# Optimization experiments

Hardware: AMD Instinct MI355X
Metric: run time of the kernel (lower is better)

## Reference

```python
import jax, jax.numpy as jnp
import numpy as np

E, M, T, H, V = 512, 1024, 1024, 512, 10000
B, S, L = 16, 80, 200
K = 10  # pooling kernel


def avgpool2d(x, k):
    # torch AvgPool2d(k) on a 3D tensor [B, S, C]: pools over (S, C) with stride k, floor mode
    b, s, c = x.shape
    return x[:, :(s // k) * k, :(c // k) * k].reshape(b, s // k, k, c // k, k).mean(axis=(2, 4))


def lstm(x, h0, c0, Wih, Whh, bih, bhh):
    # torch single-layer LSTM, gate order (i, f, g, o); x: [B, T, H]
    def step(carry, xt):
        h, c = carry
        g = xt @ Wih.T + h @ Whh.T + bih + bhh  # [B, 4H]
        i, f, gg, o = jnp.split(g, 4, axis=-1)
        c = jax.nn.sigmoid(f) * c + jax.nn.sigmoid(i) * jnp.tanh(gg)
        h = jax.nn.sigmoid(o) * jnp.tanh(c)
        return (h, c), h
    (hT, cT), ys = jax.lax.scan(step, (h0, c0), jnp.swapaxes(x, 0, 1))
    return jnp.swapaxes(ys, 0, 1), (hT, cT)


def attend(emb, feats, lens, Ws, bs, hdim):
    # additive score: Linear(cat(emb, feat)) = emb@We.T + feat@Wf.T + b, masked softmax over valid feats
    we, wf = Ws[:, :hdim], Ws[:, hdim:]
    scores = emb @ we.T + jnp.swapaxes(feats @ wf.T, 1, 2) + bs  # [B, S, L]
    mask = jnp.arange(feats.shape[1])[None, None, :] < lens[:, None, None]
    w = jax.nn.softmax(jnp.where(mask, scores, -jnp.inf), axis=-1)
    return jnp.einsum('bsl,blf->bsf', w, feats)


def setup_inputs():
    key = jax.random.key(0)
    ks = jax.random.split(key, 30)
    n = lambda k, shape: jax.random.normal(k, shape, dtype=jnp.float32)
    p = lambda k, shape: 0.02 * jax.random.normal(k, shape, dtype=jnp.float32)
    inp = {
        'mfeat': n(ks[0], (B, L, M)),
        'tfeat': n(ks[1], (B, L, T)),
        'att_motion': n(ks[2], (B, S, M)),
        'att_tempo': n(ks[3], (B, S, T)),
        'embeddings': n(ks[4], (B, S, E)),
        'motion_batch_lens': jax.random.randint(ks[5], (B,), 100, L + 1, dtype=jnp.int32),
        'temp_batch_lens': jax.random.randint(ks[6], (B,), 100, L + 1, dtype=jnp.int32),
        'seq_batch_lens': jnp.full((B,), S, dtype=jnp.int32),
        'Wm': p(ks[7], (M, M)), 'bm': p(ks[8], (M,)),
        'Wt': p(ks[9], (T, T)), 'bt': p(ks[10], (T,)),
        'Wmm': p(ks[11], (H, E + T + M)), 'bmm': p(ks[12], (H,)),
        'Wli': p(ks[13], (H, T // K + M // K)), 'bli': p(ks[14], (H,)),
        'Wih': p(ks[15], (4 * H, H)), 'Whh': p(ks[16], (4 * H, H)),
        'bih': p(ks[17], (4 * H,)), 'bhh': p(ks[18], (4 * H,)),
        'Wsm': p(ks[19], (1, H + M)), 'bsm': p(ks[20], (1,)),
        'Wst': p(ks[21], (1, H + T)), 'bst': p(ks[22], (1,)),
        'Wo': p(ks[23], (V, H + T + M)), 'bo': p(ks[24], (V,)),
    }
    return inp


def reference(mfeat, tfeat, att_motion, att_tempo, embeddings,
              motion_batch_lens, temp_batch_lens, seq_batch_lens,
              Wm, bm, Wt, bt, Wmm, bmm, Wli, bli,
              Wih, Whh, bih, bhh, Wsm, bsm, Wst, bst, Wo, bo):
    # self-gated feature transforms
    temp_mout = att_motion @ Wm.T + bm
    temp_tout = att_tempo @ Wt.T + bt
    temp_mout = temp_mout * jax.nn.softmax(temp_mout, axis=-1)
    temp_tout = temp_tout * jax.nn.softmax(temp_tout, axis=-1)
    # multimodal fusion (dropout = identity in eval)
    mm_inp = jnp.concatenate((embeddings, temp_tout, temp_mout), axis=2)
    mm_out = mm_inp @ Wmm.T + bmm  # [B, S, H]
    # pooled init sequence -> LSTM init hidden
    mean_feat = jnp.concatenate((avgpool2d(att_tempo, K), avgpool2d(att_motion, K)), axis=2)
    m0 = mean_feat @ Wli.T + bli  # [B, S//K, H]
    z = jnp.zeros((att_motion.shape[0], H), dtype=mm_out.dtype)
    _, (h0, c0) = lstm(m0, z, z, Wih, Whh, bih, bhh)
    out, _ = lstm(mm_out, h0, c0, Wih, Whh, bih, bhh)
    act = jnp.tanh(out)
    # ragged additive attention over variable-length video features
    att_m2 = attend(act, mfeat, motion_batch_lens, Wsm, bsm, H)
    att_t2 = attend(act, tfeat, temp_batch_lens, Wst, bst, H)
    final = jnp.concatenate((act, att_t2, att_m2), axis=2) @ Wo.T + bo
    return jax.nn.log_softmax(final, axis=2)
```

## Files before the change

kernel.cpp:

```cpp
#include <hip/hip_runtime.h>
#include <hip/hip_bf16.h>
#include <math.h>


typedef __bf16 bf16x8 __attribute__((ext_vector_type(8)));
typedef float f32x4 __attribute__((ext_vector_type(4)));
typedef unsigned short u16x8 __attribute__((ext_vector_type(8)));

__device__ inline unsigned short f2b(float f){
  union { float f; unsigned u; } v; v.f = f;
  unsigned u = v.u;
  u += 0x7fff + ((u >> 16) & 1);
  return (unsigned short)(u >> 16);
}
__device__ inline float sigm(float x){ return 1.f/(1.f + __expf(-x)); }
__device__ inline float wred_max(float v){ for (int o=32;o;o>>=1) v = fmaxf(v, __shfl_xor(v,o)); return v; }
__device__ inline float wred_sum(float v){ for (int o=32;o;o>>=1) v += __shfl_xor(v,o); return v; }

__device__ inline float bred_max(float v, float* sm){
  v = wred_max(v);
  int w = threadIdx.x >> 6;
  if ((threadIdx.x & 63) == 0) sm[w] = v;
  __syncthreads();
  v = fmaxf(fmaxf(sm[0], sm[1]), fmaxf(sm[2], sm[3]));
  __syncthreads();
  return v;
}
__device__ inline float bred_sum(float v, float* sm){
  v = wred_sum(v);
  int w = threadIdx.x >> 6;
  if ((threadIdx.x & 63) == 0) sm[w] = v;
  __syncthreads();
  v = sm[0] + sm[1] + sm[2] + sm[3];
  __syncthreads();
  return v;
}

#define GLOAD_LDS16(g, l) __builtin_amdgcn_global_load_lds( \
    (const __attribute__((address_space(1))) void*)(g), \
    (__attribute__((address_space(3))) void*)(l), 16, 0, 0)

__global__ void cvt_bf16_kernel(const float* __restrict__ s, unsigned short* __restrict__ d, int n8){
  int i = blockIdx.x*256 + threadIdx.x;
  if (i >= n8) return;
  float4 a = ((const float4*)s)[i*2];
  float4 b = ((const float4*)s)[i*2+1];
  u16x8 o;
  o[0]=f2b(a.x); o[1]=f2b(a.y); o[2]=f2b(a.z); o[3]=f2b(a.w);
  o[4]=f2b(b.x); o[5]=f2b(b.y); o[6]=f2b(b.z); o[7]=f2b(b.w);
  ((u16x8*)d)[i] = o;
}

__global__ void zero_kernel(int* p, int n){
  int i = blockIdx.x*64 + threadIdx.x;
  if (i < n) p[i] = 0;
}

__device__ __forceinline__ void gemm_body(
    const unsigned short* __restrict__ A, const unsigned short* __restrict__ B,
    const float* __restrict__ bias1, const float* __restrict__ bias2,
    float* __restrict__ C, int N, int K,
    unsigned short* lA, unsigned short* lB)
{
  int tid = threadIdx.x;
  int r0 = blockIdx.x << 7, n0 = blockIdx.y << 7;
  int w = tid >> 6, lane = tid & 63;
  int wr = (w >> 1) << 6, wc = (w & 1) << 6;
  int lm = lane & 15, lq = lane >> 4;
  f32x4 acc[4][4] = {};

  int row0 = tid >> 2, row1 = (tid + 256) >> 2, cc = (tid & 3) << 3;
  const unsigned short* Ag0 = A + (size_t)(r0 + row0)*K + cc;
  const unsigned short* Ag1 = A + (size_t)(r0 + row1)*K + cc;
  int br0 = n0 + row0; if (br0 >= N) br0 = N - 1;
  int br1 = n0 + row1; if (br1 >= N) br1 = N - 1;
  const unsigned short* Bg0 = B + (size_t)br0*K + cc;
  const unsigned short* Bg1 = B + (size_t)br1*K + cc;
  unsigned lb0 = (unsigned)(tid & ~63) * 8;
  unsigned lb1 = 2048 + lb0;

  for (int k0 = 0; k0 < K; k0 += 32){
    GLOAD_LDS16(Ag0 + k0, &lA[lb0]);
    GLOAD_LDS16(Ag1 + k0, &lA[lb1]);
    GLOAD_LDS16(Bg0 + k0, &lB[lb0]);
    GLOAD_LDS16(Bg1 + k0, &lB[lb1]);
    __syncthreads();
    bf16x8 af[4], bfr[4];
#pragma unroll
    for (int i=0;i<4;i++){
      af[i]  = *(const bf16x8*)&lA[(wr + i*16 + lm)*32 + lq*8];
      bfr[i] = *(const bf16x8*)&lB[(wc + i*16 + lm)*32 + lq*8];
    }
#pragma unroll
    for (int i=0;i<4;i++)
#pragma unroll
      for (int j=0;j<4;j++)
        acc[i][j] = __builtin_amdgcn_mfma_f32_16x16x32_bf16(af[i], bfr[j], acc[i][j], 0, 0, 0);
    __syncthreads();
  }
#pragma unroll
  for (int i=0;i<4;i++){
    int rbase = r0 + wr + i*16 + lq*4;
#pragma unroll
    for (int j=0;j<4;j++){
      int n = n0 + wc + j*16 + lm;
      if (n < N){
        float bv = (bias1 ? bias1[n] : 0.f) + (bias2 ? bias2[n] : 0.f);
#pragma unroll
        for (int rr=0;rr<4;rr++)
          C[(size_t)(rbase + rr)*N + n] = acc[i][j][rr] + bv;
      }
    }
  }
}

__global__ __launch_bounds__(256) void gemm_bb_kernel(
    const unsigned short* __restrict__ A, const unsigned short* __restrict__ B,
    const float* __restrict__ bias1, const float* __restrict__ bias2,
    float* __restrict__ C, int N, int K)
{
  __shared__ unsigned short lA[128*32];
  __shared__ unsigned short lB[128*32];
  gemm_body(A, B, bias1, bias2, C, N, K, lA, lB);
}

__global__ __launch_bounds__(256) void gemm_bb2_kernel(
    const unsigned short* __restrict__ A0, const unsigned short* __restrict__ B0,
    const float* __restrict__ b0, float* __restrict__ C0,
    const unsigned short* __restrict__ A1, const unsigned short* __restrict__ B1,
    const float* __restrict__ b1, float* __restrict__ C1, int N, int K)
{
  __shared__ unsigned short lA[128*32];
  __shared__ unsigned short lB[128*32];
  if (blockIdx.z == 0) gemm_body(A0, B0, b0, nullptr, C0, N, K, lA, lB);
  else                 gemm_body(A1, B1, b1, nullptr, C1, N, K, lA, lB);
}

__global__ __launch_bounds__(256) void rowsmx2_kernel(const float* __restrict__ X0,
    const float* __restrict__ X1, unsigned short* __restrict__ out)
{
  __shared__ float sm[4];
  int bx = blockIdx.x, tid = threadIdx.x;
  int row = (bx < 1280) ? bx : bx - 1280;
  const float* xr = ((bx < 1280) ? X0 : X1) + (size_t)row * 1024;
  int ooff = (bx < 1280) ? 1536 : 512;
  float x[4];
#pragma unroll
  for (int j=0;j<4;j++) x[j] = xr[j*256 + tid];
  float m = fmaxf(fmaxf(x[0],x[1]), fmaxf(x[2],x[3]));
  m = bred_max(m, sm);
  float s = 0.f;
#pragma unroll
  for (int j=0;j<4;j++) s += __expf(x[j]-m);
  s = bred_sum(s, sm);
  float inv = 1.f / s;
  unsigned short* o = out + (size_t)row*2560 + ooff;
#pragma unroll
  for (int j=0;j<4;j++) o[j*256 + tid] = f2b(x[j] * (__expf(x[j]-m) * inv));
}

__global__ void embcopy_kernel(const float* __restrict__ emb, unsigned short* __restrict__ mmbf){
  int idx = blockIdx.x*256 + threadIdx.x;
  if (idx >= 1280*64) return;
  int row = idx >> 6, c8 = (idx & 63) << 3;
  const float* s = emb + (size_t)row*512 + c8;
  float4 a = ((const float4*)s)[0], b = ((const float4*)s)[1];
  u16x8 o;
  o[0]=f2b(a.x); o[1]=f2b(a.y); o[2]=f2b(a.z); o[3]=f2b(a.w);
  o[4]=f2b(b.x); o[5]=f2b(b.y); o[6]=f2b(b.z); o[7]=f2b(b.w);
  *(u16x8*)&mmbf[(size_t)row*2560 + c8] = o;
}

__global__ void avgpool_kernel(const float* __restrict__ tempo, const float* __restrict__ motion,
                               float* __restrict__ mf)
{
  int bx = blockIdx.x;
  int c = threadIdx.x;
  if (c >= 204) return;
  int b = bx >> 3, s = bx & 7;
  const float* src = (c < 102) ? (tempo  + ((size_t)(b*80 + s*10))*1024 + c*10)
                               : (motion + ((size_t)(b*80 + s*10))*1024 + (c-102)*10);
  float acc = 0.f;
  for (int r=0;r<10;r++){
    const float* p = src + (size_t)r*1024;
#pragma unroll
    for (int cc=0;cc<10;cc++) acc += p[cc];
  }
  mf[bx*204 + c] = acc * 0.01f;
}

__global__ __launch_bounds__(256) void m0_kernel(const float* __restrict__ mf,
    const float* __restrict__ Wli, const float* __restrict__ bli, float* __restrict__ m0)
{
  __shared__ float rowv[204];
  int bx = blockIdx.x, tid = threadIdx.x;
  if (tid < 204) rowv[tid] = mf[bx*204 + tid];
  __syncthreads();
  for (int c = tid; c < 512; c += 256){
    const float* w = Wli + (size_t)c*204;
    float acc = bli[c];
    for (int k=0;k<204;k++) acc += rowv[k]*w[k];
    m0[bx*512 + c] = acc;
  }
}

#define LSTM_NBLK 32
#define HP 520

__global__ __launch_bounds__(256) void lstm_fused_kernel(
    const float* __restrict__ X1, const float* __restrict__ X2,
    const float* __restrict__ Whh,
    unsigned long long* __restrict__ hb0, unsigned long long* __restrict__ hb1,
    float* __restrict__ finalA, unsigned short* __restrict__ finalA_bf,
    int* __restrict__ bar,
    const float* __restrict__ Wo, unsigned short* __restrict__ Wo_bf,
    const float* __restrict__ mfeat, const float* __restrict__ tfeat,
    const float* __restrict__ Wsm, const float* __restrict__ Wst,
    float* __restrict__ f_m, float* __restrict__ f_t)
{
  __shared__ unsigned short w_lds[64*HP];
  __shared__ unsigned short h_lds[16*HP];
  __shared__ float gb[4][16][16];
  __shared__ unsigned short hstage[16][16];
  int tid = threadIdx.x, j = blockIdx.x;

  if (j >= LSTM_NBLK){
    int hb = j - LSTM_NBLK;
    for (int ch = hb*256 + tid; ch < 3200000; ch += 224*256){
      float4 a = ((const float4*)Wo)[ch*2];
      float4 b = ((const float4*)Wo)[ch*2+1];
      u16x8 o;
      o[0]=f2b(a.x); o[1]=f2b(a.y); o[2]=f2b(a.z); o[3]=f2b(a.w);
      o[4]=f2b(b.x); o[5]=f2b(b.y); o[6]=f2b(b.z); o[7]=f2b(b.w);
      ((u16x8*)Wo_bf)[ch] = o;
    }
    int wv = hb*4 + (tid >> 6);
    int lane = tid & 63;
    for (int r = wv; r < 6400; r += 896){
      const float* a = (r < 3200) ? (mfeat + (size_t)r*1024) : (tfeat + (size_t)(r-3200)*1024);
      const float* wvec = (r < 3200) ? (Wsm + 512) : (Wst + 512);
      float acc = 0.f;
      for (int c = lane; c < 1024; c += 64) acc += a[c]*wvec[c];
      acc = wred_sum(acc);
      if (lane == 0){ if (r < 3200) f_m[r] = acc; else f_t[r-3200] = acc; }
    }
    return;
  }

  int j16 = j*16;
  int lane = tid & 63, w = tid >> 6;
  int lm = lane & 15, lq = lane >> 4;

  for (int i = 0; i < 16; i++){
    int ch = tid + i*256;
    int r = ch >> 6, c8 = (ch & 63) << 3;
    int grow = (r >> 4)*512 + j16 + (r & 15);
    const float* s = Whh + (size_t)grow*512 + c8;
    float4 a = ((const float4*)s)[0], b = ((const float4*)s)[1];
    u16x8 o;
    o[0]=f2b(a.x); o[1]=f2b(a.y); o[2]=f2b(a.z); o[3]=f2b(a.w);
    o[4]=f2b(b.x); o[5]=f2b(b.y); o[6]=f2b(b.z); o[7]=f2b(b.w);
    *(u16x8*)&w_lds[r*HP + c8] = o;
  }

  float c_reg = 0.f;
  int ul = tid & 15, bb = tid >> 4;
  unsigned long long* hbufs[2] = { hb0, hb1 };
  const int wbase = ((w << 4) + lm)*HP;
  const int abase = lm*HP;
  const int koff = lq << 3;
  int sc = 0;

  for (int seg = 0; seg < 2; seg++){
    const float* Xp = seg ? X2 : X1;
    int Tst = seg ? 80 : 8;
    for (int t = 0; t < Tst; t++){
      if (sc > 0){
        if (tid == 0){
          while (__hip_atomic_load(&bar[sc-1], __ATOMIC_RELAXED, __HIP_MEMORY_SCOPE_AGENT) < LSTM_NBLK)
            __builtin_amdgcn_s_sleep(1);
        }
        __syncthreads();
      }
      size_t xrow = ((size_t)bb*Tst + t)*2048 + j16 + ul;
      float xi = Xp[xrow];
      float xf = Xp[xrow + 512];
      float xg = Xp[xrow + 1024];
      float xo = Xp[xrow + 1536];
      if (sc == 0){
        u16x8 z = {0,0,0,0,0,0,0,0};
        for (int i = tid; i < 1024; i += 256){
          int b = i >> 6, c8 = (i & 63) << 3;
          *(u16x8*)&h_lds[b*HP + c8] = z;
        }
      } else {
        const unsigned long long* src = hbufs[sc & 1];
#pragma unroll
        for (int it = 0; it < 8; it++){
          int i = tid + it*256;
          int b = i >> 7, c64 = i & 127;
          unsigned long long v = __hip_atomic_load(&src[i], __ATOMIC_RELAXED, __HIP_MEMORY_SCOPE_AGENT);
          *(unsigned long long*)&h_lds[b*HP + (c64 << 2)] = v;
        }
      }
      __syncthreads();
      f32x4 a0 = {0.f,0.f,0.f,0.f}, a1 = {0.f,0.f,0.f,0.f};
#pragma unroll
      for (int k0 = 0; k0 < 512; k0 += 64){
        bf16x8 ha = *(const bf16x8*)&h_lds[abase + k0 + koff];
        bf16x8 wa = *(const bf16x8*)&w_lds[wbase + k0 + koff];
        a0 = __builtin_amdgcn_mfma_f32_16x16x32_bf16(ha, wa, a0, 0, 0, 0);
        bf16x8 hbf = *(const bf16x8*)&h_lds[abase + k0 + 32 + koff];
        bf16x8 wbf = *(const bf16x8*)&w_lds[wbase + k0 + 32 + koff];
        a1 = __builtin_amdgcn_mfma_f32_16x16x32_bf16(hbf, wbf, a1, 0, 0, 0);
      }
      f32x4 acc = a0 + a1;
      *(f32x4*)&gb[w][lm][lq << 2] = acc;
      __syncthreads();
      float iv = gb[0][ul][bb] + xi;
      float fv = gb[1][ul][bb] + xf;
      float gv = gb[2][ul][bb] + xg;
      float ov = gb[3][ul][bb] + xo;
      c_reg = sigm(fv)*c_reg + sigm(iv)*tanhf(gv);
      float hn = sigm(ov)*tanhf(c_reg);
      hstage[bb][ul] = f2b(hn);
      if (seg){
        float act = tanhf(hn);
        size_t fo = (size_t)(bb*80 + t)*2560 + j16 + ul;
        finalA[fo] = act;
        finalA_bf[fo] = f2b(act);
      }
      __syncthreads();
      if (tid < 64){
        int b = tid >> 2, ch = tid & 3;
        unsigned long long v = *(const unsigned long long*)&hstage[b][ch << 2];
        unsigned long long* dst = hbufs[(sc + 1) & 1] + (size_t)b*128 + (j << 2) + ch;
        __hip_atomic_store(dst, v, __ATOMIC_RELAXED, __HIP_MEMORY_SCOPE_AGENT);
      }
      sc++;
      __syncthreads();
      if (tid == 0)
        __hip_atomic_fetch_add(&bar[sc-1], 1, __ATOMIC_RELAXED, __HIP_MEMORY_SCOPE_AGENT);
    }
  }
}

__global__ void proj_kernel(const float* __restrict__ A, int stride, int ncols,
                            const float* __restrict__ w, const float* __restrict__ bias,
                            float* __restrict__ out)
{
  int r = blockIdx.x, lane = threadIdx.x;
  const float* a = A + (size_t)r * stride;
  float acc = 0.f;
  for (int c = lane; c < ncols; c += 64) acc += a[c]*w[c];
  acc = wred_sum(acc);
  if (lane == 0) out[r] = acc + (bias ? bias[0] : 0.f);
}

__global__ __launch_bounds__(256) void attsmax_kernel(const float* __restrict__ e,
    const float* __restrict__ f, const int* __restrict__ lens, float* __restrict__ w)
{
  __shared__ float sm[4];
  int bx = blockIdx.x;
  int b = bx / 80;
  int tid = threadIdx.x;
  int len = lens[b];
  bool ok = (tid < 200) && (tid < len);
  float val = ok ? (e[bx] + f[b*200 + tid]) : -1e30f;
  float m = bred_max(val, sm);
  float ex = ok ? __expf(val - m) : 0.f;
  float s = bred_sum(ex, sm);
  if (tid < 200) w[(size_t)bx*200 + tid] = ex / s;
}

__global__ __launch_bounds__(256) void attapply_kernel(const float* __restrict__ w,
    const float* __restrict__ feats, unsigned short* __restrict__ finalA_bf, int coloff)
{
  __shared__ float lw[8][200];
  int b = blockIdx.x, sg = blockIdx.y;
  int tid = threadIdx.x;
  for (int i = tid; i < 1600; i += 256){
    int ss = i / 200, l = i - ss*200;
    lw[ss][l] = w[(size_t)(b*80 + sg*8 + ss)*200 + l];
  }
  __syncthreads();
  float4 acc[8];
#pragma unroll
  for (int s=0;s<8;s++) acc[s] = make_float4(0,0,0,0);
  const float* fb = feats + (size_t)b*200*1024 + tid*4;
  for (int l=0;l<200;l++){
    float4 v = *(const float4*)(fb + (size_t)l*1024);
#pragma unroll
    for (int s=0;s<8;s++){
      float wv = lw[s][l];
      acc[s].x += wv*v.x; acc[s].y += wv*v.y; acc[s].z += wv*v.z; acc[s].w += wv*v.w;
    }
  }
#pragma unroll
  for (int s=0;s<8;s++){
    ushort4 o;
    o.x = f2b(acc[s].x); o.y = f2b(acc[s].y); o.z = f2b(acc[s].z); o.w = f2b(acc[s].w);
    *(ushort4*)&finalA_bf[(size_t)(b*80 + sg*8 + s)*2560 + coloff + tid*4] = o;
  }
}

__global__ __launch_bounds__(256) void logsmax_kernel(float* __restrict__ out)
{
  __shared__ float buf[10000];
  __shared__ float sm[4];
  int row = blockIdx.x, tid = threadIdx.x;
  float* o = out + (size_t)row * 10000;
  float m = -1e30f;
  for (int i = tid; i < 10000; i += 256){ float v = o[i]; buf[i] = v; m = fmaxf(m, v); }
  m = bred_max(m, sm);
  float s = 0.f;
  for (int i = tid; i < 10000; i += 256) s += __expf(buf[i] - m);
  s = bred_sum(s, sm);
  float lse = m + __logf(s);
  for (int i = tid; i < 10000; i += 256) o[i] = buf[i] - lse;
}

extern "C" void kernel_launch(void* const* d_in, const int* in_sizes, int n_in,
                              void* d_out, int out_size, void* d_ws, size_t ws_size,
                              hipStream_t stream)
{
  const float* mfeat = (const float*)d_in[0];
  const float* tfeat = (const float*)d_in[1];
  const float* attm  = (const float*)d_in[2];
  const float* attt  = (const float*)d_in[3];
  const float* emb   = (const float*)d_in[4];
  const int* lens_m  = (const int*)d_in[5];
  const int* lens_t  = (const int*)d_in[6];
  const float* Wm  = (const float*)d_in[8];
  const float* bm  = (const float*)d_in[9];
  const float* Wt  = (const float*)d_in[10];
  const float* bt  = (const float*)d_in[11];
  const float* Wmm = (const float*)d_in[12];
  const float* bmm = (const float*)d_in[13];
  const float* Wli = (const float*)d_in[14];
  const float* bli = (const float*)d_in[15];
  const float* Wih = (const float*)d_in[16];
  const float* Whh = (const float*)d_in[17];
  const float* bih = (const float*)d_in[18];
  const float* bhh = (const float*)d_in[19];
  const float* Wsm = (const float*)d_in[20];
  const float* bsm = (const float*)d_in[21];
  const float* Wst = (const float*)d_in[22];
  const float* bst = (const float*)d_in[23];
  const float* Wo  = (const float*)d_in[24];
  const float* bo  = (const float*)d_in[25];
  float* out = (float*)d_out;

  char* ws = (char*)d_ws;
  size_t off = 0;
  auto alloc = [&](size_t bytes)->void* {
    void* p = (void*)(ws + off);
    off += (bytes + 255) & ~(size_t)255;
    return p;
  };
  float* finalA = (float*)alloc(1280UL*2560*4);
  float* moutp  = (float*)alloc(1280UL*1024*4);
  float* toutp  = (float*)alloc(1280UL*1024*4);
  float* mm_out = (float*)alloc(1280UL*512*4);
  float* meanf  = (float*)alloc(128UL*204*4);
  float* m0     = (float*)alloc(128UL*512*4);
  float* X1     = (float*)alloc(128UL*2048*4);
  float* X2     = (float*)alloc(1280UL*2048*4);
  float* e_m = (float*)alloc(1280UL*4); float* e_t = (float*)alloc(1280UL*4);
  float* f_m = (float*)alloc(3200UL*4); float* f_t = (float*)alloc(3200UL*4);
  float* w_m = (float*)alloc(1280UL*200*4); float* w_t = (float*)alloc(1280UL*200*4);
  int* bar = (int*)alloc(128*4);
  unsigned long long* hbuf0 = (unsigned long long*)alloc(16UL*128*8);
  unsigned long long* hbuf1 = (unsigned long long*)alloc(16UL*128*8);
  unsigned short* attm_bf   = (unsigned short*)alloc(1280UL*1024*2);
  unsigned short* attt_bf   = (unsigned short*)alloc(1280UL*1024*2);
  unsigned short* Wm_bf     = (unsigned short*)alloc(1024UL*1024*2);
  unsigned short* Wt_bf     = (unsigned short*)alloc(1024UL*1024*2);
  unsigned short* Wmm_bf    = (unsigned short*)alloc(512UL*2560*2);
  unsigned short* Wih_bf    = (unsigned short*)alloc(2048UL*512*2);
  unsigned short* Wo_bf     = (unsigned short*)alloc(10000UL*2560*2);
  unsigned short* mm_inp_bf = (unsigned short*)alloc(1280UL*2560*2);
  unsigned short* mm_out_bf = (unsigned short*)alloc(1280UL*512*2);
  unsigned short* m0_bf     = (unsigned short*)alloc(128UL*512*2);
  unsigned short* finalA_bf = (unsigned short*)alloc(1280UL*2560*2);

  auto cvt = [&](const float* s, unsigned short* d, size_t n){
    int n8 = (int)(n/8);
    cvt_bf16_kernel<<<(n8 + 255)/256, 256, 0, stream>>>(s, d, n8);
  };
  cvt(attm, attm_bf, 1280UL*1024);
  cvt(attt, attt_bf, 1280UL*1024);
  cvt(Wm,  Wm_bf,  1024UL*1024);
  cvt(Wt,  Wt_bf,  1024UL*1024);
  cvt(Wmm, Wmm_bf, 512UL*2560);
  cvt(Wih, Wih_bf, 2048UL*512);
  zero_kernel<<<2, 64, 0, stream>>>(bar, 128);

  gemm_bb2_kernel<<<dim3(10, 8, 2), 256, 0, stream>>>(
      attm_bf, Wm_bf, bm, moutp, attt_bf, Wt_bf, bt, toutp, 1024, 1024);
  rowsmx2_kernel<<<2560, 256, 0, stream>>>(moutp, toutp, mm_inp_bf);
  embcopy_kernel<<<(1280*64 + 255)/256, 256, 0, stream>>>(emb, mm_inp_bf);
  gemm_bb_kernel<<<dim3(10, 4), 256, 0, stream>>>(mm_inp_bf, Wmm_bf, bmm, nullptr, mm_out, 512, 2560);
  cvt(mm_out, mm_out_bf, 1280UL*512);
  avgpool_kernel<<<128, 256, 0, stream>>>(attt, attm, meanf);
  m0_kernel<<<128, 256, 0, stream>>>(meanf, Wli, bli, m0);
  cvt(m0, m0_bf, 128UL*512);
  gemm_bb_kernel<<<dim3(1, 16), 256, 0, stream>>>(m0_bf, Wih_bf, bih, bhh, X1, 2048, 512);
  gemm_bb_kernel<<<dim3(10, 16), 256, 0, stream>>>(mm_out_bf, Wih_bf, bih, bhh, X2, 2048, 512);
  lstm_fused_kernel<<<256, 256, 0, stream>>>(X1, X2, Whh, hbuf0, hbuf1,
      finalA, finalA_bf, bar, Wo, Wo_bf, mfeat, tfeat, Wsm, Wst, f_m, f_t);
  proj_kernel<<<1280, 64, 0, stream>>>(finalA, 2560, 512, Wsm, bsm, e_m);
  proj_kernel<<<1280, 64, 0, stream>>>(finalA, 2560, 512, Wst, bst, e_t);
  attsmax_kernel<<<1280, 256, 0, stream>>>(e_t, f_t, lens_t, w_t);
  attsmax_kernel<<<1280, 256, 0, stream>>>(e_m, f_m, lens_m, w_m);
  attapply_kernel<<<dim3(16,10), 256, 0, stream>>>(w_t, tfeat, finalA_bf, 512);
  attapply_kernel<<<dim3(16,10), 256, 0, stream>>>(w_m, mfeat, finalA_bf, 1536);
  gemm_bb_kernel<<<dim3(10, 79), 256, 0, stream>>>(finalA_bf, Wo_bf, bo, nullptr, out, 10000, 2560);
  logsmax_kernel<<<1280, 256, 0, stream>>>(out);
}
```

Before: 1.028 ms.

## Fuse conversion, pooling, projection and attention kernels; cut launches and fp32 roundtrips

Merges the six bf16 conversions plus the embedding copy into one launch, fuses avgpool with the m0 projection writing bf16, has GEMMs emit bf16 directly, merges the X1/X2 input GEMMs, and combines projection with masked softmax and both attention directions into single launches. The LSTM now uses an exp-based tanh, moves the finalA writes after the barrier signal, and reads Wo with nontemporal loads. The aim is to remove launch overhead and intermediate fp32 traffic. The fast tanh may lose a little accuracy.

```diff
diff --git a/kernel.cpp b/kernel.cpp
--- a/kernel.cpp
+++ b/kernel.cpp
@@ -14,6 +14,10 @@
   return (unsigned short)(u >> 16);
 }
 __device__ inline float sigm(float x){ return 1.f/(1.f + __expf(-x)); }
+__device__ inline float tanh_fast(float x){
+  float e = __expf(2.f*x);
+  return 1.f - 2.f/(e + 1.f);
+}
 __device__ inline float wred_max(float v){ for (int o=32;o;o>>=1) v = fmaxf(v, __shfl_xor(v,o)); return v; }
 __device__ inline float wred_sum(float v){ for (int o=32;o;o>>=1) v += __shfl_xor(v,o); return v; }
 
@@ -40,30 +44,54 @@
     (const __attribute__((address_space(1))) void*)(g), \
     (__attribute__((address_space(3))) void*)(l), 16, 0, 0)
 
-__global__ void cvt_bf16_kernel(const float* __restrict__ s, unsigned short* __restrict__ d, int n8){
-  int i = blockIdx.x*256 + threadIdx.x;
-  if (i >= n8) return;
-  float4 a = ((const float4*)s)[i*2];
-  float4 b = ((const float4*)s)[i*2+1];
-  u16x8 o;
-  o[0]=f2b(a.x); o[1]=f2b(a.y); o[2]=f2b(a.z); o[3]=f2b(a.w);
-  o[4]=f2b(b.x); o[5]=f2b(b.y); o[6]=f2b(b.z); o[7]=f2b(b.w);
-  ((u16x8*)d)[i] = o;
-}
-
 __global__ void zero_kernel(int* p, int n){
   int i = blockIdx.x*64 + threadIdx.x;
   if (i < n) p[i] = 0;
 }
 
+__global__ void cvt7_kernel(
+    const float* __restrict__ attm, const float* __restrict__ attt,
+    const float* __restrict__ Wm,   const float* __restrict__ Wt,
+    const float* __restrict__ Wmm,  const float* __restrict__ Wih,
+    const float* __restrict__ emb,
+    unsigned short* __restrict__ attm_bf, unsigned short* __restrict__ attt_bf,
+    unsigned short* __restrict__ Wm_bf,   unsigned short* __restrict__ Wt_bf,
+    unsigned short* __restrict__ Wmm_bf,  unsigned short* __restrict__ Wih_bf,
+    unsigned short* __restrict__ mm_inp_bf)
+{
+  int i = blockIdx.x*256 + threadIdx.x;
+  const float* s; unsigned short* d; int o;
+  if (i < 458752){
+    if (i < 163840){ s = attm; d = attm_bf; o = i; }
+    else if (i < 327680){ s = attt; d = attt_bf; o = i - 163840; }
+    else { s = Wm; d = Wm_bf; o = i - 327680; }
+  } else if (i < 753664){
+    if (i < 589824){ s = Wt; d = Wt_bf; o = i - 458752; }
+    else { s = Wmm; d = Wmm_bf; o = i - 589824; }
+  } else {
+    if (i < 884736){ s = Wih; d = Wih_bf; o = i - 753664; }
+    else { s = emb; d = mm_inp_bf; o = i - 884736; }
+  }
+  f32x4 a = ((const f32x4*)s)[(size_t)o*2];
+  f32x4 b = ((const f32x4*)s)[(size_t)o*2+1];
+  u16x8 v;
+  v[0]=f2b(a[0]); v[1]=f2b(a[1]); v[2]=f2b(a[2]); v[3]=f2b(a[3]);
+  v[4]=f2b(b[0]); v[5]=f2b(b[1]); v[6]=f2b(b[2]); v[7]=f2b(b[3]);
+  if (i >= 884736){
+    int row = o >> 6, c8 = (o & 63) << 3;
+    *(u16x8*)&d[(size_t)row*2560 + c8] = v;
+  } else {
+    ((u16x8*)d)[o] = v;
+  }
+}
+
 __device__ __forceinline__ void gemm_body(
     const unsigned short* __restrict__ A, const unsigned short* __restrict__ B,
     const float* __restrict__ bias1, const float* __restrict__ bias2,
-    float* __restrict__ C, int N, int K,
-    unsigned short* lA, unsigned short* lB)
+    float* __restrict__ C, unsigned short* __restrict__ Cbf, int N, int K,
+    unsigned short* lA, unsigned short* lB, int r0, int n0)
 {
   int tid = threadIdx.x;
-  int r0 = blockIdx.x << 7, n0 = blockIdx.y << 7;
   int w = tid >> 6, lane = tid & 63;
   int wr = (w >> 1) << 6, wc = (w & 1) << 6;
   int lm = lane & 15, lq = lane >> 4;
@@ -106,9 +134,15 @@
       int n = n0 + wc + j*16 + lm;
       if (n < N){
         float bv = (bias1 ? bias1[n] : 0.f) + (bias2 ? bias2[n] : 0.f);
-#pragma unroll
-        for (int rr=0;rr<4;rr++)
-          C[(size_t)(rbase + rr)*N + n] = acc[i][j][rr] + bv;
+        if (Cbf){
+#pragma unroll
+          for (int rr=0;rr<4;rr++)
+            Cbf[(size_t)(rbase + rr)*N + n] = f2b(acc[i][j][rr] + bv);
+        } else {
+#pragma unroll
+          for (int rr=0;rr<4;rr++)
+            C[(size_t)(rbase + rr)*N + n] = acc[i][j][rr] + bv;
+        }
       }
     }
   }
@@ -117,11 +151,11 @@
 __global__ __launch_bounds__(256) void gemm_bb_kernel(
     const unsigned short* __restrict__ A, const unsigned short* __restrict__ B,
     const float* __restrict__ bias1, const float* __restrict__ bias2,
-    float* __restrict__ C, int N, int K)
+    float* __restrict__ C, unsigned short* __restrict__ Cbf, int N, int K)
 {
   __shared__ unsigned short lA[128*32];
   __shared__ unsigned short lB[128*32];
-  gemm_body(A, B, bias1, bias2, C, N, K, lA, lB);
+  gemm_body(A, B, bias1, bias2, C, Cbf, N, K, lA, lB, blockIdx.x << 7, blockIdx.y << 7);
 }
 
 __global__ __launch_bounds__(256) void gemm_bb2_kernel(
@@ -132,8 +166,22 @@
 {
   __shared__ unsigned short lA[128*32];
   __shared__ unsigned short lB[128*32];
-  if (blockIdx.z == 0) gemm_body(A0, B0, b0, nullptr, C0, N, K, lA, lB);
-  else                 gemm_body(A1, B1, b1, nullptr, C1, N, K, lA, lB);
+  if (blockIdx.z == 0) gemm_body(A0, B0, b0, nullptr, C0, nullptr, N, K, lA, lB, blockIdx.x << 7, blockIdx.y << 7);
+  else                 gemm_body(A1, B1, b1, nullptr, C1, nullptr, N, K, lA, lB, blockIdx.x << 7, blockIdx.y << 7);
+}
+
+__global__ __launch_bounds__(256) void gemm_x12_kernel(
+    const unsigned short* __restrict__ m0_bf, const unsigned short* __restrict__ mmo_bf,
+    const unsigned short* __restrict__ Wih_bf,
+    const float* __restrict__ bih, const float* __restrict__ bhh,
+    float* __restrict__ X1, float* __restrict__ X2)
+{
+  __shared__ unsigned short lA[128*32];
+  __shared__ unsigned short lB[128*32];
+  if (blockIdx.x == 0)
+    gemm_body(m0_bf, Wih_bf, bih, bhh, X1, nullptr, 2048, 512, lA, lB, 0, blockIdx.y << 7);
+  else
+    gemm_body(mmo_bf, Wih_bf, bih, bhh, X2, nullptr, 2048, 512, lA, lB, (blockIdx.x - 1) << 7, blockIdx.y << 7);
 }
 
 __global__ __launch_bounds__(256) void rowsmx2_kernel(const float* __restrict__ X0,
@@ -159,48 +207,32 @@
   for (int j=0;j<4;j++) o[j*256 + tid] = f2b(x[j] * (__expf(x[j]-m) * inv));
 }
 
-__global__ void embcopy_kernel(const float* __restrict__ emb, unsigned short* __restrict__ mmbf){
-  int idx = blockIdx.x*256 + threadIdx.x;
-  if (idx >= 1280*64) return;
-  int row = idx >> 6, c8 = (idx & 63) << 3;
-  const float* s = emb + (size_t)row*512 + c8;
-  float4 a = ((const float4*)s)[0], b = ((const float4*)s)[1];
-  u16x8 o;
-  o[0]=f2b(a.x); o[1]=f2b(a.y); o[2]=f2b(a.z); o[3]=f2b(a.w);
-  o[4]=f2b(b.x); o[5]=f2b(b.y); o[6]=f2b(b.z); o[7]=f2b(b.w);
-  *(u16x8*)&mmbf[(size_t)row*2560 + c8] = o;
-}
-
-__global__ void avgpool_kernel(const float* __restrict__ tempo, const float* __restrict__ motion,
-                               float* __restrict__ mf)
-{
-  int bx = blockIdx.x;
-  int c = threadIdx.x;
-  if (c >= 204) return;
-  int b = bx >> 3, s = bx & 7;
-  const float* src = (c < 102) ? (tempo  + ((size_t)(b*80 + s*10))*1024 + c*10)
-                               : (motion + ((size_t)(b*80 + s*10))*1024 + (c-102)*10);
-  float acc = 0.f;
-  for (int r=0;r<10;r++){
-    const float* p = src + (size_t)r*1024;
-#pragma unroll
-    for (int cc=0;cc<10;cc++) acc += p[cc];
-  }
-  mf[bx*204 + c] = acc * 0.01f;
-}
-
-__global__ __launch_bounds__(256) void m0_kernel(const float* __restrict__ mf,
-    const float* __restrict__ Wli, const float* __restrict__ bli, float* __restrict__ m0)
+__global__ __launch_bounds__(256) void m0fused_kernel(
+    const float* __restrict__ tempo, const float* __restrict__ motion,
+    const float* __restrict__ Wli, const float* __restrict__ bli,
+    unsigned short* __restrict__ m0_bf)
 {
   __shared__ float rowv[204];
   int bx = blockIdx.x, tid = threadIdx.x;
-  if (tid < 204) rowv[tid] = mf[bx*204 + tid];
+  int b = bx >> 3, s = bx & 7;
+  if (tid < 204){
+    int c = tid;
+    const float* src = (c < 102) ? (tempo  + ((size_t)(b*80 + s*10))*1024 + c*10)
+                                 : (motion + ((size_t)(b*80 + s*10))*1024 + (c-102)*10);
+    float acc = 0.f;
+    for (int r=0;r<10;r++){
+      const float* p = src + (size_t)r*1024;
+#pragma unroll
+      for (int cc=0;cc<10;cc++) acc += p[cc];
+    }
+    rowv[c] = acc * 0.01f;
+  }
   __syncthreads();
   for (int c = tid; c < 512; c += 256){
     const float* w = Wli + (size_t)c*204;
     float acc = bli[c];
     for (int k=0;k<204;k++) acc += rowv[k]*w[k];
-    m0[bx*512 + c] = acc;
+    m0_bf[(size_t)bx*512 + c] = f2b(acc);
   }
 }
 
@@ -226,12 +258,13 @@
 
   if (j >= LSTM_NBLK){
     int hb = j - LSTM_NBLK;
+    const f32x4* wp = (const f32x4*)Wo;
     for (int ch = hb*256 + tid; ch < 3200000; ch += 224*256){
-      float4 a = ((const float4*)Wo)[ch*2];
-      float4 b = ((const float4*)Wo)[ch*2+1];
+      f32x4 a = __builtin_nontemporal_load(wp + (size_t)ch*2);
+      f32x4 b = __builtin_nontemporal_load(wp + (size_t)ch*2 + 1);
       u16x8 o;
-      o[0]=f2b(a.x); o[1]=f2b(a.y); o[2]=f2b(a.z); o[3]=f2b(a.w);
-      o[4]=f2b(b.x); o[5]=f2b(b.y); o[6]=f2b(b.z); o[7]=f2b(b.w);
+      o[0]=f2b(a[0]); o[1]=f2b(a[1]); o[2]=f2b(a[2]); o[3]=f2b(a[3]);
+      o[4]=f2b(b[0]); o[5]=f2b(b[1]); o[6]=f2b(b[2]); o[7]=f2b(b[3]);
       ((u16x8*)Wo_bf)[ch] = o;
     }
     int wv = hb*4 + (tid >> 6);
@@ -256,10 +289,10 @@
     int r = ch >> 6, c8 = (ch & 63) << 3;
     int grow = (r >> 4)*512 + j16 + (r & 15);
     const float* s = Whh + (size_t)grow*512 + c8;
-    float4 a = ((const float4*)s)[0], b = ((const float4*)s)[1];
+    f32x4 a = ((const f32x4*)s)[0], b = ((const f32x4*)s)[1];
     u16x8 o;
-    o[0]=f2b(a.x); o[1]=f2b(a.y); o[2]=f2b(a.z); o[3]=f2b(a.w);
-    o[4]=f2b(b.x); o[5]=f2b(b.y); o[6]=f2b(b.z); o[7]=f2b(b.w);
+    o[0]=f2b(a[0]); o[1]=f2b(a[1]); o[2]=f2b(a[2]); o[3]=f2b(a[3]);
+    o[4]=f2b(b[0]); o[5]=f2b(b[1]); o[6]=f2b(b[2]); o[7]=f2b(b[3]);
     *(u16x8*)&w_lds[r*HP + c8] = o;
   }
 
@@ -321,15 +354,9 @@
       float fv = gb[1][ul][bb] + xf;
       float gv = gb[2][ul][bb] + xg;
       float ov = gb[3][ul][bb] + xo;
-      c_reg = sigm(fv)*c_reg + sigm(iv)*tanhf(gv);
-      float hn = sigm(ov)*tanhf(c_reg);
+      c_reg = sigm(fv)*c_reg + sigm(iv)*tanh_fast(gv);
+      float hn = sigm(ov)*tanh_fast(c_reg);
       hstage[bb][ul] = f2b(hn);
-      if (seg){
-        float act = tanhf(hn);
-        size_t fo = (size_t)(bb*80 + t)*2560 + j16 + ul;
-        finalA[fo] = act;
-        finalA_bf[fo] = f2b(act);
-      }
       __syncthreads();
       if (tid < 64){
         int b = tid >> 2, ch = tid & 3;
@@ -341,43 +368,55 @@
       __syncthreads();
       if (tid == 0)
         __hip_atomic_fetch_add(&bar[sc-1], 1, __ATOMIC_RELAXED, __HIP_MEMORY_SCOPE_AGENT);
-    }
-  }
-}
-
-__global__ void proj_kernel(const float* __restrict__ A, int stride, int ncols,
-                            const float* __restrict__ w, const float* __restrict__ bias,
-                            float* __restrict__ out)
-{
-  int r = blockIdx.x, lane = threadIdx.x;
-  const float* a = A + (size_t)r * stride;
-  float acc = 0.f;
-  for (int c = lane; c < ncols; c += 64) acc += a[c]*w[c];
-  acc = wred_sum(acc);
-  if (lane == 0) out[r] = acc + (bias ? bias[0] : 0.f);
-}
-
-__global__ __launch_bounds__(256) void attsmax_kernel(const float* __restrict__ e,
-    const float* __restrict__ f, const int* __restrict__ lens, float* __restrict__ w)
+      if (seg){
+        float act = tanh_fast(hn);
+        size_t fo = (size_t)(bb*80 + t)*2560 + j16 + ul;
+        finalA[fo] = act;
+        finalA_bf[fo] = f2b(act);
+      }
+    }
+  }
+}
+
+__global__ __launch_bounds__(256) void attscore_kernel(const float* __restrict__ finalA,
+    const float* __restrict__ Wsm, const float* __restrict__ bsm,
+    const float* __restrict__ Wst, const float* __restrict__ bst,
+    const float* __restrict__ f_m, const float* __restrict__ f_t,
+    const int* __restrict__ lens_m, const int* __restrict__ lens_t,
+    float* __restrict__ w_m, float* __restrict__ w_t)
 {
   __shared__ float sm[4];
-  int bx = blockIdx.x;
-  int b = bx / 80;
-  int tid = threadIdx.x;
+  int bx = blockIdx.x, tid = threadIdx.x;
+  bool mside = bx >= 1280;
+  int row = mside ? bx - 1280 : bx;
+  const float* wv = mside ? Wsm : Wst;
+  float bias = (mside ? bsm : bst)[0];
+  const float* f = mside ? f_m : f_t;
+  const int* lens = mside ? lens_m : lens_t;
+  float* w = mside ? w_m : w_t;
+  const float* a = finalA + (size_t)row*2560;
+  float d = a[tid]*wv[tid] + a[256+tid]*wv[256+tid];
+  float e = bred_sum(d, sm) + bias;
+  int b = row/80;
   int len = lens[b];
   bool ok = (tid < 200) && (tid < len);
-  float val = ok ? (e[bx] + f[b*200 + tid]) : -1e30f;
+  float val = ok ? (e + f[b*200 + tid]) : -1e30f;
   float m = bred_max(val, sm);
   float ex = ok ? __expf(val - m) : 0.f;
   float s = bred_sum(ex, sm);
-  if (tid < 200) w[(size_t)bx*200 + tid] = ex / s;
-}
-
-__global__ __launch_bounds__(256) void attapply_kernel(const float* __restrict__ w,
-    const float* __restrict__ feats, unsigned short* __restrict__ finalA_bf, int coloff)
+  if (tid < 200) w[(size_t)row*200 + tid] = ex / s;
+}
+
+__global__ __launch_bounds__(256) void attapply_kernel(
+    const float* __restrict__ w_t, const float* __restrict__ w_m,
+    const float* __restrict__ tfeat, const float* __restrict__ mfeat,
+    unsigned short* __restrict__ finalA_bf)
 {
   __shared__ float lw[8][200];
-  int b = blockIdx.x, sg = blockIdx.y;
+  int b = blockIdx.x, sg = blockIdx.y, z = blockIdx.z;
+  const float* w = z ? w_m : w_t;
+  const float* feats = z ? mfeat : tfeat;
+  int coloff = z ? 1536 : 512;
   int tid = threadIdx.x;
   for (int i = tid; i < 1600; i += 256){
     int ss = i / 200, l = i - ss*200;
@@ -461,12 +500,8 @@
   float* finalA = (float*)alloc(1280UL*2560*4);
   float* moutp  = (float*)alloc(1280UL*1024*4);
   float* toutp  = (float*)alloc(1280UL*1024*4);
-  float* mm_out = (float*)alloc(1280UL*512*4);
-  float* meanf  = (float*)alloc(128UL*204*4);
-  float* m0     = (float*)alloc(128UL*512*4);
   float* X1     = (float*)alloc(128UL*2048*4);
   float* X2     = (float*)alloc(1280UL*2048*4);
-  float* e_m = (float*)alloc(1280UL*4); float* e_t = (float*)alloc(1280UL*4);
   float* f_m = (float*)alloc(3200UL*4); float* f_t = (float*)alloc(3200UL*4);
   float* w_m = (float*)alloc(1280UL*200*4); float* w_t = (float*)alloc(1280UL*200*4);
   int* bar = (int*)alloc(128*4);
@@ -484,37 +519,23 @@
   unsigned short* m0_bf     = (unsigned short*)alloc(128UL*512*2);
   unsigned short* finalA_bf = (unsigned short*)alloc(1280UL*2560*2);
 
-  auto cvt = [&](const float* s, unsigned short* d, size_t n){
-    int n8 = (int)(n/8);
-    cvt_bf16_kernel<<<(n8 + 255)/256, 256, 0, stream>>>(s, d, n8);
-  };
-  cvt(attm, attm_bf, 1280UL*1024);
-  cvt(attt, attt_bf, 1280UL*1024);
-  cvt(Wm,  Wm_bf,  1024UL*1024);
-  cvt(Wt,  Wt_bf,  1024UL*1024);
-  cvt(Wmm, Wmm_bf, 512UL*2560);
-  cvt(Wih, Wih_bf, 2048UL*512);
+  cvt7_kernel<<<3776, 256, 0, stream>>>(attm, attt, Wm, Wt, Wmm, Wih, emb,
+      attm_bf, attt_bf, Wm_bf, Wt_bf, Wmm_bf, Wih_bf, mm_inp_bf);
   zero_kernel<<<2, 64, 0, stream>>>(bar, 128);
 
   gemm_bb2_kernel<<<dim3(10, 8, 2), 256, 0, stream>>>(
       attm_bf, Wm_bf, bm, moutp, attt_bf, Wt_bf, bt, toutp, 1024, 1024);
   rowsmx2_kernel<<<2560, 256, 0, stream>>>(moutp, toutp, mm_inp_bf);
-  embcopy_kernel<<<(1280*64 + 255)/256, 256, 0, stream>>>(emb, mm_inp_bf);
-  gemm_bb_kernel<<<dim3(10, 4), 256, 0, stream>>>(mm_inp_bf, Wmm_bf, bmm, nullptr, mm_out, 512, 2560);
-  cvt(mm_out, mm_out_bf, 1280UL*512);
-  avgpool_kernel<<<128, 256, 0, stream>>>(attt, attm, meanf);
-  m0_kernel<<<128, 256, 0, stream>>>(meanf, Wli, bli, m0);
-  cvt(m0, m0_bf, 128UL*512);
-  gemm_bb_kernel<<<dim3(1, 16), 256, 0, stream>>>(m0_bf, Wih_bf, bih, bhh, X1, 2048, 512);
-  gemm_bb_kernel<<<dim3(10, 16), 256, 0, stream>>>(mm_out_bf, Wih_bf, bih, bhh, X2, 2048, 512);
+  gemm_bb_kernel<<<dim3(10, 4), 256, 0, stream>>>(mm_inp_bf, Wmm_bf, bmm, nullptr,
+      nullptr, mm_out_bf, 512, 2560);
+  m0fused_kernel<<<128, 256, 0, stream>>>(attt, attm, Wli, bli, m0_bf);
+  gemm_x12_kernel<<<dim3(11, 16), 256, 0, stream>>>(m0_bf, mm_out_bf, Wih_bf, bih, bhh, X1, X2);
   lstm_fused_kernel<<<256, 256, 0, stream>>>(X1, X2, Whh, hbuf0, hbuf1,
       finalA, finalA_bf, bar, Wo, Wo_bf, mfeat, tfeat, Wsm, Wst, f_m, f_t);
-  proj_kernel<<<1280, 64, 0, stream>>>(finalA, 2560, 512, Wsm, bsm, e_m);
-  proj_kernel<<<1280, 64, 0, stream>>>(finalA, 2560, 512, Wst, bst, e_t);
-  attsmax_kernel<<<1280, 256, 0, stream>>>(e_t, f_t, lens_t, w_t);
-  attsmax_kernel<<<1280, 256, 0, stream>>>(e_m, f_m, lens_m, w_m);
-  attapply_kernel<<<dim3(16,10), 256, 0, stream>>>(w_t, tfeat, finalA_bf, 512);
-  attapply_kernel<<<dim3(16,10), 256, 0, stream>>>(w_m, mfeat, finalA_bf, 1536);
-  gemm_bb_kernel<<<dim3(10, 79), 256, 0, stream>>>(finalA_bf, Wo_bf, bo, nullptr, out, 10000, 2560);
+  attscore_kernel<<<2560, 256, 0, stream>>>(finalA, Wsm, bsm, Wst, bst,
+      f_m, f_t, lens_m, lens_t, w_m, w_t);
+  attapply_kernel<<<dim3(16, 10, 2), 256, 0, stream>>>(w_t, w_m, tfeat, mfeat, finalA_bf);
+  gemm_bb_kernel<<<dim3(10, 79), 256, 0, stream>>>(finalA_bf, Wo_bf, bo, nullptr,
+      out, nullptr, 10000, 2560);
   logsmax_kernel<<<1280, 256, 0, stream>>>(out);
 }
```

After: 925.7 us. 9.9% less time.
